# Kernel optimization log

Measured on AMD Instinct MI355X. Metric: run time of the kernel, lower is better.

Reference implementation:

```python
import jax, jax.numpy as jnp
import numpy as np

MASK_VALUE = 0.0  # default `mask=0` scalar in the original forward


def setup_inputs() -> dict:
    key = jax.random.key(0)
    kq, kk, kv = jax.random.split(key, 3)
    b, n, d_k, d_v = 8, 2048, 64, 64
    q = jax.random.normal(kq, (b, n, d_k), dtype=jnp.float32)
    k = jax.random.normal(kk, (b, n, d_k), dtype=jnp.float32)
    v = jax.random.normal(kv, (b, n, d_v), dtype=jnp.float32)
    return {"q": q, "k": k, "v": v}


def reference(q, k, v):
    d_k = q.shape[-1]
    temper = jnp.asarray(d_k, q.dtype) ** 0.5
    # scores: (b, n, n)
    attn = jnp.einsum('bqd,bkd->bqk', q, k) / temper
    # equality-based masking: positions whose score exactly equals the
    # scalar `mask` (default 0) are set to -inf before softmax.
    attn = jnp.where(attn == MASK_VALUE, -jnp.inf, attn)
    # NOTE: the original code calls `attn.masked_fill(look_ahead_mask==0, -inf)`
    # WITHOUT assignment, so the look-ahead mask is a no-op; we omit it faithfully.
    attn = jax.nn.softmax(attn, axis=-1)
    out = jnp.einsum('bqk,bkd->bqd', attn, v)  # (b, n, d_v)
    return out
```

## Files before the change

### kernel.cpp

```cpp
#include <hip/hip_runtime.h>
#include <hip/hip_bf16.h>

typedef __bf16 bf16_t;
typedef bf16_t bf16x2 __attribute__((ext_vector_type(2)));
typedef bf16_t bf16x8 __attribute__((ext_vector_type(8)));
typedef float  floatx4  __attribute__((ext_vector_type(4)));
typedef float  floatx16 __attribute__((ext_vector_type(16)));
typedef int    intx2    __attribute__((ext_vector_type(2)));

constexpr int B = 8, N = 2048, D = 64;

__global__ __launch_bounds__(256)
void prepass_kernel(const float* __restrict__ k, const float* __restrict__ v,
                    bf16_t* __restrict__ kf, bf16_t* __restrict__ vf) {
    __shared__ float t[32 * 65];
    const int tid = threadIdx.x;
    const int b   = blockIdx.x & 7;
    const int kvb = blockIdx.x >> 3;
    const size_t inoff  = ((size_t)b * N + kvb * 32) * D;
    const size_t outoff = (size_t)(b * 64 + kvb) * 2048;

    {
        const float* src = k + inoff;
        floatx4 f0 = *(const floatx4*)(src + tid * 8);
        floatx4 f1 = *(const floatx4*)(src + tid * 8 + 4);
        bf16x8 o;
        #pragma unroll
        for (int j = 0; j < 4; ++j) { o[j] = (bf16_t)f0[j]; o[j + 4] = (bf16_t)f1[j]; }
        const int rr = tid >> 3, kd = (tid >> 1) & 3, hh = tid & 1;
        *(bf16x8*)(kf + outoff + (size_t)kd * 512 + (hh * 32 + rr) * 8) = o;
    }
    {
        const float* src = v + inoff;
        floatx4 f0 = *(const floatx4*)(src + tid * 8);
        floatx4 f1 = *(const floatx4*)(src + tid * 8 + 4);
        const int rr = tid >> 3, cc = (tid & 7) * 8;
        #pragma unroll
        for (int j = 0; j < 4; ++j) { t[rr * 65 + cc + j] = f0[j]; t[rr * 65 + cc + 4 + j] = f1[j]; }
        __syncthreads();
        const int s2 = tid >> 7, dblk = (tid >> 6) & 1, lane = tid & 63;
        const int hh = lane >> 5, l31 = lane & 31;
        bf16x8 o;
        #pragma unroll
        for (int j = 0; j < 8; ++j)
            o[j] = (bf16_t)t[(s2 * 16 + hh * 8 + j) * 65 + dblk * 32 + l31];
        *(bf16x8*)(vf + outoff + (size_t)(s2 * 2 + dblk) * 512 + lane * 8) = o;
    }
}

__global__ __launch_bounds__(512, 4)
void attn_kernel(const float* __restrict__ q, const bf16_t* __restrict__ kf,
                 const bf16_t* __restrict__ vf, float* __restrict__ out) {
    __shared__ float o_buf[8 * 2048];
    __shared__ float l_buf[8 * 32];

    const int tid  = threadIdx.x;
    const int lane = tid & 63;
    const int cg   = tid >> 6;
    const int h    = lane >> 5;
    const int l31  = lane & 31;

    const int b  = blockIdx.x & 7;
    const int q0 = (blockIdx.x >> 3) * 32;

    const bf16_t* kfb = kf + (size_t)b * 131072;
    const bf16_t* vfb = vf + (size_t)b * 131072;

    constexpr float QSCALE = 0.125f * 1.4426950408889634f;
    bf16x8 qf[4];
    {
        const float* qp = q + ((size_t)b * N + q0 + l31) * D + h * 8;
        #pragma unroll
        for (int kd = 0; kd < 4; ++kd) {
            floatx4 f0 = *(const floatx4*)(qp + kd * 16);
            floatx4 f1 = *(const floatx4*)(qp + kd * 16 + 4);
            bf16x8 t;
            #pragma unroll
            for (int j = 0; j < 4; ++j) {
                t[j]     = (bf16_t)(f0[j] * QSCALE);
                t[j + 4] = (bf16_t)(f1[j] * QSCALE);
            }
            qf[kd] = t;
        }
    }

    floatx16 o_acc[2];
    #pragma unroll
    for (int d = 0; d < 2; ++d)
        #pragma unroll
        for (int i = 0; i < 16; ++i) o_acc[d][i] = 0.f;
    float l_run0 = 0.f, l_run1 = 0.f;

    bf16x8 kreg[4];
    #pragma unroll
    for (int kd = 0; kd < 4; ++kd)
        kreg[kd] = *(const bf16x8*)(kfb + (size_t)cg * 2048 + kd * 512 + lane * 8);

    #pragma unroll 2
    for (int it = 0; it < 8; ++it) {
        const size_t base = (size_t)(it * 8 + cg) * 2048;

        bf16x8 vreg[4];
        #pragma unroll
        for (int u = 0; u < 4; ++u)
            vreg[u] = *(const bf16x8*)(vfb + base + (size_t)u * 512 + lane * 8);

        floatx16 s;
        #pragma unroll
        for (int i = 0; i < 16; ++i) s[i] = 0.f;
        __builtin_amdgcn_s_setprio(1);
        #pragma unroll
        for (int kd = 0; kd < 4; ++kd)
            s = __builtin_amdgcn_mfma_f32_32x32x16_bf16(kreg[kd], qf[kd], s, 0, 0, 0);
        __builtin_amdgcn_s_setprio(0);

        if (it + 1 < 8) {
            const size_t nbase = (size_t)((it + 1) * 8 + cg) * 2048;
            #pragma unroll
            for (int kd = 0; kd < 4; ++kd)
                kreg[kd] = *(const bf16x8*)(kfb + nbase + (size_t)kd * 512 + lane * 8);
        }

        int q8[8];
        #pragma unroll
        for (int g = 0; g < 8; ++g) {
            union { int i; bf16x2 h2; } u;
            {
                float x = s[2 * g + 0];
                float p = (x == 0.0f) ? 0.0f : __builtin_amdgcn_exp2f(x);
                l_run0 += p;
                u.h2[0] = (bf16_t)p;
            }
            {
                float x = s[2 * g + 1];
                float p = (x == 0.0f) ? 0.0f : __builtin_amdgcn_exp2f(x);
                l_run1 += p;
                u.h2[1] = (bf16_t)p;
            }
            q8[g] = u.i;
        }

        #pragma unroll
        for (int s2 = 0; s2 < 2; ++s2) {
            intx2 p02 = __builtin_amdgcn_permlane32_swap(q8[4 * s2 + 0], q8[4 * s2 + 2], false, false);
            intx2 p13 = __builtin_amdgcn_permlane32_swap(q8[4 * s2 + 1], q8[4 * s2 + 3], false, false);
            union { int i4[4]; bf16x8 v; } bf;
            bf.i4[0] = p02[0];
            bf.i4[1] = p13[0];
            bf.i4[2] = p02[1];
            bf.i4[3] = p13[1];
            __builtin_amdgcn_s_setprio(1);
            #pragma unroll
            for (int dblk = 0; dblk < 2; ++dblk)
                o_acc[dblk] = __builtin_amdgcn_mfma_f32_32x32x16_bf16(vreg[s2 * 2 + dblk], bf.v,
                                                                      o_acc[dblk], 0, 0, 0);
            __builtin_amdgcn_s_setprio(0);
        }
    }

    float l_run = l_run0 + l_run1;
    l_run += __shfl_xor(l_run, 32);

    {
        float* ob = o_buf + cg * 2048;
        #pragma unroll
        for (int dblk = 0; dblk < 2; ++dblk)
            #pragma unroll
            for (int i = 0; i < 16; ++i) {
                const int d = (i & 3) + 8 * (i >> 2) + 4 * h + dblk * 32;
                ob[d * 32 + l31] = o_acc[dblk][i];
            }
        if (h == 0) l_buf[cg * 32 + l31] = l_run;
    }
    __syncthreads();
    {
        const int dblk = cg >> 2, g = cg & 3;
        const int d0 = 8 * g + 4 * h + dblk * 32;
        float lsum = 0.f;
        #pragma unroll
        for (int w = 0; w < 8; ++w) lsum += l_buf[w * 32 + l31];
        const float inv_l = 1.0f / lsum;
        floatx4 o4;
        #pragma unroll
        for (int j = 0; j < 4; ++j) {
            float sum = 0.f;
            #pragma unroll
            for (int w = 0; w < 8; ++w) sum += o_buf[w * 2048 + (d0 + j) * 32 + l31];
            o4[j] = sum * inv_l;
        }
        *(floatx4*)(out + ((size_t)b * N + q0 + l31) * D + d0) = o4;
    }
}

extern "C" void kernel_launch(void* const* d_in, const int* in_sizes, int n_in,
                              void* d_out, int out_size, void* d_ws, size_t ws_size,
                              hipStream_t stream) {
    const float* q = (const float*)d_in[0];
    const float* k = (const float*)d_in[1];
    const float* v = (const float*)d_in[2];
    float* out = (float*)d_out;
    bf16_t* kfrag = (bf16_t*)d_ws;
    bf16_t* vfrag = (bf16_t*)((char*)d_ws + (size_t)B * N * D * 2);

    hipLaunchKernelGGL(prepass_kernel, dim3(512), dim3(256), 0, stream, k, v, kfrag, vfrag);
    hipLaunchKernelGGL(attn_kernel, dim3(512), dim3(512), 0, stream, q, kfrag, vfrag, out);
}
```

Measured before the change: 80.68 us.

## Stream K/V tiles through LDS double buffer with global_load_lds and 4 waves

```diff
diff --git a/kernel.cpp b/kernel.cpp
--- a/kernel.cpp
+++ b/kernel.cpp
@@ -9,6 +9,12 @@
 typedef int    intx2    __attribute__((ext_vector_type(2)));
 
 constexpr int B = 8, N = 2048, D = 64;
+
+typedef __attribute__((address_space(1))) const void gconst_t;
+typedef __attribute__((address_space(3))) void lds_t;
+__device__ __forceinline__ void gload_lds16(const void* g, void* l) {
+    __builtin_amdgcn_global_load_lds((gconst_t*)g, (lds_t*)l, 16, 0, 0);
+}
 
 __global__ __launch_bounds__(256)
 void prepass_kernel(const float* __restrict__ k, const float* __restrict__ v,
@@ -48,11 +54,10 @@
     }
 }
 
-__global__ __launch_bounds__(512, 4)
+__global__ __launch_bounds__(256, 2)
 void attn_kernel(const float* __restrict__ q, const bf16_t* __restrict__ kf,
                  const bf16_t* __restrict__ vf, float* __restrict__ out) {
-    __shared__ float o_buf[8 * 2048];
-    __shared__ float l_buf[8 * 32];
+    __shared__ __align__(16) char smem[65536];
 
     const int tid  = threadIdx.x;
     const int lane = tid & 63;
@@ -63,8 +68,9 @@
     const int b  = blockIdx.x & 7;
     const int q0 = (blockIdx.x >> 3) * 32;
 
-    const bf16_t* kfb = kf + (size_t)b * 131072;
-    const bf16_t* vfb = vf + (size_t)b * 131072;
+    const char* kfb = (const char*)(kf + (size_t)b * 131072);
+    const char* vfb = (const char*)(vf + (size_t)b * 131072);
+    char* ring = smem + cg * 16384;
 
     constexpr float QSCALE = 0.125f * 1.4426950408889634f;
     bf16x8 qf[4];
@@ -84,6 +90,16 @@
         }
     }
 
+    {
+        const char* kc = kfb + (size_t)cg * 4096;
+        const char* vc = vfb + (size_t)cg * 4096;
+        #pragma unroll
+        for (int j = 0; j < 4; ++j) {
+            gload_lds16(kc + j * 1024 + lane * 16, ring + j * 1024);
+            gload_lds16(vc + j * 1024 + lane * 16, ring + 4096 + j * 1024);
+        }
+    }
+
     floatx16 o_acc[2];
     #pragma unroll
     for (int d = 0; d < 2; ++d)
@@ -91,19 +107,30 @@
         for (int i = 0; i < 16; ++i) o_acc[d][i] = 0.f;
     float l_run0 = 0.f, l_run1 = 0.f;
 
-    bf16x8 kreg[4];
     #pragma unroll
-    for (int kd = 0; kd < 4; ++kd)
-        kreg[kd] = *(const bf16x8*)(kfb + (size_t)cg * 2048 + kd * 512 + lane * 8);
-
-    #pragma unroll 2
-    for (int it = 0; it < 8; ++it) {
-        const size_t base = (size_t)(it * 8 + cg) * 2048;
-
-        bf16x8 vreg[4];
-        #pragma unroll
-        for (int u = 0; u < 4; ++u)
-            vreg[u] = *(const bf16x8*)(vfb + base + (size_t)u * 512 + lane * 8);
+    for (int it = 0; it < 16; ++it) {
+        char* cur = ring + (it & 1) * 8192;
+
+        if (it < 15) {
+            char* nxt = ring + ((it + 1) & 1) * 8192;
+            const char* kc = kfb + (size_t)((it + 1) * 4 + cg) * 4096;
+            const char* vc = vfb + (size_t)((it + 1) * 4 + cg) * 4096;
+            #pragma unroll
+            for (int j = 0; j < 4; ++j) {
+                gload_lds16(kc + j * 1024 + lane * 16, nxt + j * 1024);
+                gload_lds16(vc + j * 1024 + lane * 16, nxt + 4096 + j * 1024);
+            }
+            asm volatile("s_waitcnt vmcnt(8)" ::: "memory");
+        } else {
+            asm volatile("s_waitcnt vmcnt(0)" ::: "memory");
+        }
+
+        bf16x8 kreg[4], vreg[4];
+        #pragma unroll
+        for (int kd = 0; kd < 4; ++kd) {
+            kreg[kd] = *(const bf16x8*)(cur + kd * 1024 + lane * 16);
+            vreg[kd] = *(const bf16x8*)(cur + 4096 + kd * 1024 + lane * 16);
+        }
 
         floatx16 s;
         #pragma unroll
@@ -113,13 +140,6 @@
         for (int kd = 0; kd < 4; ++kd)
             s = __builtin_amdgcn_mfma_f32_32x32x16_bf16(kreg[kd], qf[kd], s, 0, 0, 0);
         __builtin_amdgcn_s_setprio(0);
-
-        if (it + 1 < 8) {
-            const size_t nbase = (size_t)((it + 1) * 8 + cg) * 2048;
-            #pragma unroll
-            for (int kd = 0; kd < 4; ++kd)
-                kreg[kd] = *(const bf16x8*)(kfb + nbase + (size_t)kd * 512 + lane * 8);
-        }
 
         int q8[8];
         #pragma unroll
@@ -162,7 +182,7 @@
     l_run += __shfl_xor(l_run, 32);
 
     {
-        float* ob = o_buf + cg * 2048;
+        float* ob = (float*)ring;
         #pragma unroll
         for (int dblk = 0; dblk < 2; ++dblk)
             #pragma unroll
@@ -170,25 +190,31 @@
                 const int d = (i & 3) + 8 * (i >> 2) + 4 * h + dblk * 32;
                 ob[d * 32 + l31] = o_acc[dblk][i];
             }
-        if (h == 0) l_buf[cg * 32 + l31] = l_run;
+        if (h == 0) ((float*)(ring + 8192))[l31] = l_run;
     }
     __syncthreads();
     {
-        const int dblk = cg >> 2, g = cg & 3;
-        const int d0 = 8 * g + 4 * h + dblk * 32;
+        const int mdblk = cg & 1;
+        const int g0 = (cg >> 1) * 2;
         float lsum = 0.f;
         #pragma unroll
-        for (int w = 0; w < 8; ++w) lsum += l_buf[w * 32 + l31];
+        for (int w = 0; w < 4; ++w) lsum += ((const float*)(smem + w * 16384 + 8192))[l31];
         const float inv_l = 1.0f / lsum;
-        floatx4 o4;
-        #pragma unroll
-        for (int j = 0; j < 4; ++j) {
-            float sum = 0.f;
-            #pragma unroll
-            for (int w = 0; w < 8; ++w) sum += o_buf[w * 2048 + (d0 + j) * 32 + l31];
-            o4[j] = sum * inv_l;
-        }
-        *(floatx4*)(out + ((size_t)b * N + q0 + l31) * D + d0) = o4;
+        float* op = out + ((size_t)b * N + q0 + l31) * D;
+        #pragma unroll
+        for (int gg = 0; gg < 2; ++gg) {
+            const int d0 = 8 * (g0 + gg) + 4 * h + mdblk * 32;
+            floatx4 o4;
+            #pragma unroll
+            for (int j = 0; j < 4; ++j) {
+                float sum = 0.f;
+                #pragma unroll
+                for (int w = 0; w < 4; ++w)
+                    sum += ((const float*)(smem + w * 16384))[(d0 + j) * 32 + l31];
+                o4[j] = sum * inv_l;
+            }
+            *(floatx4*)(op + d0) = o4;
+        }
     }
 }
 
@@ -203,5 +229,5 @@
     bf16_t* vfrag = (bf16_t*)((char*)d_ws + (size_t)B * N * D * 2);
 
     hipLaunchKernelGGL(prepass_kernel, dim3(512), dim3(256), 0, stream, k, v, kfrag, vfrag);
-    hipLaunchKernelGGL(attn_kernel, dim3(512), dim3(512), 0, stream, q, kfrag, vfrag, out);
-}
+    hipLaunchKernelGGL(attn_kernel, dim3(512), dim3(256), 0, stream, q, kfrag, vfrag, out);
+}
```

Measured after the change: 82.29 us. 1.02x slower.

## Process two 32-row query tiles per block to reuse K/V fragment loads

Applied to the files above, without the earlier changes.

```diff
diff --git a/kernel.cpp b/kernel.cpp
--- a/kernel.cpp
+++ b/kernel.cpp
@@ -48,11 +48,10 @@
     }
 }
 
-__global__ __launch_bounds__(512, 4)
+__global__ __launch_bounds__(512, 2)
 void attn_kernel(const float* __restrict__ q, const bf16_t* __restrict__ kf,
                  const bf16_t* __restrict__ vf, float* __restrict__ out) {
     __shared__ float o_buf[8 * 2048];
-    __shared__ float l_buf[8 * 32];
 
     const int tid  = threadIdx.x;
     const int lane = tid & 63;
@@ -61,35 +60,38 @@
     const int l31  = lane & 31;
 
     const int b  = blockIdx.x & 7;
-    const int q0 = (blockIdx.x >> 3) * 32;
+    const int q0 = (blockIdx.x >> 3) * 64;
 
     const bf16_t* kfb = kf + (size_t)b * 131072;
     const bf16_t* vfb = vf + (size_t)b * 131072;
 
     constexpr float QSCALE = 0.125f * 1.4426950408889634f;
-    bf16x8 qf[4];
-    {
-        const float* qp = q + ((size_t)b * N + q0 + l31) * D + h * 8;
+    bf16x8 qf[2][4];
+    #pragma unroll
+    for (int t = 0; t < 2; ++t) {
+        const float* qp = q + ((size_t)b * N + q0 + t * 32 + l31) * D + h * 8;
         #pragma unroll
         for (int kd = 0; kd < 4; ++kd) {
             floatx4 f0 = *(const floatx4*)(qp + kd * 16);
             floatx4 f1 = *(const floatx4*)(qp + kd * 16 + 4);
-            bf16x8 t;
+            bf16x8 tt;
             #pragma unroll
             for (int j = 0; j < 4; ++j) {
-                t[j]     = (bf16_t)(f0[j] * QSCALE);
-                t[j + 4] = (bf16_t)(f1[j] * QSCALE);
-            }
-            qf[kd] = t;
-        }
-    }
-
-    floatx16 o_acc[2];
-    #pragma unroll
-    for (int d = 0; d < 2; ++d)
-        #pragma unroll
-        for (int i = 0; i < 16; ++i) o_acc[d][i] = 0.f;
-    float l_run0 = 0.f, l_run1 = 0.f;
+                tt[j]     = (bf16_t)(f0[j] * QSCALE);
+                tt[j + 4] = (bf16_t)(f1[j] * QSCALE);
+            }
+            qf[t][kd] = tt;
+        }
+    }
+
+    floatx16 o_acc[2][2];
+    #pragma unroll
+    for (int t = 0; t < 2; ++t)
+        #pragma unroll
+        for (int d = 0; d < 2; ++d)
+            #pragma unroll
+            for (int i = 0; i < 16; ++i) o_acc[t][d][i] = 0.f;
+    float l_run[2][2] = {{0.f, 0.f}, {0.f, 0.f}};
 
     bf16x8 kreg[4];
     #pragma unroll
@@ -105,13 +107,18 @@
         for (int u = 0; u < 4; ++u)
             vreg[u] = *(const bf16x8*)(vfb + base + (size_t)u * 512 + lane * 8);
 
-        floatx16 s;
-        #pragma unroll
-        for (int i = 0; i < 16; ++i) s[i] = 0.f;
+        floatx16 s[2];
+        #pragma unroll
+        for (int t = 0; t < 2; ++t)
+            #pragma unroll
+            for (int i = 0; i < 16; ++i) s[t][i] = 0.f;
         __builtin_amdgcn_s_setprio(1);
         #pragma unroll
         for (int kd = 0; kd < 4; ++kd)
-            s = __builtin_amdgcn_mfma_f32_32x32x16_bf16(kreg[kd], qf[kd], s, 0, 0, 0);
+            s[0] = __builtin_amdgcn_mfma_f32_32x32x16_bf16(kreg[kd], qf[0][kd], s[0], 0, 0, 0);
+        #pragma unroll
+        for (int kd = 0; kd < 4; ++kd)
+            s[1] = __builtin_amdgcn_mfma_f32_32x32x16_bf16(kreg[kd], qf[1][kd], s[1], 0, 0, 0);
         __builtin_amdgcn_s_setprio(0);
 
         if (it + 1 < 8) {
@@ -121,74 +128,99 @@
                 kreg[kd] = *(const bf16x8*)(kfb + nbase + (size_t)kd * 512 + lane * 8);
         }
 
-        int q8[8];
-        #pragma unroll
-        for (int g = 0; g < 8; ++g) {
-            union { int i; bf16x2 h2; } u;
-            {
-                float x = s[2 * g + 0];
-                float p = (x == 0.0f) ? 0.0f : __builtin_amdgcn_exp2f(x);
-                l_run0 += p;
-                u.h2[0] = (bf16_t)p;
-            }
-            {
-                float x = s[2 * g + 1];
-                float p = (x == 0.0f) ? 0.0f : __builtin_amdgcn_exp2f(x);
-                l_run1 += p;
-                u.h2[1] = (bf16_t)p;
-            }
-            q8[g] = u.i;
-        }
-
-        #pragma unroll
-        for (int s2 = 0; s2 < 2; ++s2) {
-            intx2 p02 = __builtin_amdgcn_permlane32_swap(q8[4 * s2 + 0], q8[4 * s2 + 2], false, false);
-            intx2 p13 = __builtin_amdgcn_permlane32_swap(q8[4 * s2 + 1], q8[4 * s2 + 3], false, false);
-            union { int i4[4]; bf16x8 v; } bf;
-            bf.i4[0] = p02[0];
-            bf.i4[1] = p13[0];
-            bf.i4[2] = p02[1];
-            bf.i4[3] = p13[1];
-            __builtin_amdgcn_s_setprio(1);
+        #pragma unroll
+        for (int t = 0; t < 2; ++t) {
+            int q8[8];
+            #pragma unroll
+            for (int g = 0; g < 8; ++g) {
+                union { int i; bf16x2 h2; } u;
+                {
+                    float x = s[t][2 * g + 0];
+                    float p = (x == 0.0f) ? 0.0f : __builtin_amdgcn_exp2f(x);
+                    l_run[t][0] += p;
+                    u.h2[0] = (bf16_t)p;
+                }
+                {
+                    float x = s[t][2 * g + 1];
+                    float p = (x == 0.0f) ? 0.0f : __builtin_amdgcn_exp2f(x);
+                    l_run[t][1] += p;
+                    u.h2[1] = (bf16_t)p;
+                }
+                q8[g] = u.i;
+            }
+
+            #pragma unroll
+            for (int s2 = 0; s2 < 2; ++s2) {
+                intx2 p02 = __builtin_amdgcn_permlane32_swap(q8[4 * s2 + 0], q8[4 * s2 + 2], false, false);
+                intx2 p13 = __builtin_amdgcn_permlane32_swap(q8[4 * s2 + 1], q8[4 * s2 + 3], false, false);
+                union { int i4[4]; bf16x8 v; } bf;
+                bf.i4[0] = p02[0];
+                bf.i4[1] = p13[0];
+                bf.i4[2] = p02[1];
+                bf.i4[3] = p13[1];
+                __builtin_amdgcn_s_setprio(1);
+                #pragma unroll
+                for (int dblk = 0; dblk < 2; ++dblk)
+                    o_acc[t][dblk] = __builtin_amdgcn_mfma_f32_32x32x16_bf16(vreg[s2 * 2 + dblk], bf.v,
+                                                                             o_acc[t][dblk], 0, 0, 0);
+                __builtin_amdgcn_s_setprio(0);
+            }
+        }
+    }
+
+    #pragma unroll
+    for (int t = 0; t < 2; ++t) {
+        float l = l_run[t][0] + l_run[t][1];
+        l += __shfl_xor(l, 32);
+        l_run[t][0] = l;
+    }
+
+    if (h == 0) {
+        o_buf[cg * 32 + l31]       = l_run[0][0];
+        o_buf[256 + cg * 32 + l31] = l_run[1][0];
+    }
+    __syncthreads();
+    float inv_l[2];
+    {
+        float s0 = 0.f, s1 = 0.f;
+        #pragma unroll
+        for (int w = 0; w < 8; ++w) {
+            s0 += o_buf[w * 32 + l31];
+            s1 += o_buf[256 + w * 32 + l31];
+        }
+        inv_l[0] = 1.0f / s0;
+        inv_l[1] = 1.0f / s1;
+    }
+
+    #pragma unroll
+    for (int t = 0; t < 2; ++t) {
+        __syncthreads();
+        {
+            float* ob = o_buf + cg * 2048;
             #pragma unroll
             for (int dblk = 0; dblk < 2; ++dblk)
-                o_acc[dblk] = __builtin_amdgcn_mfma_f32_32x32x16_bf16(vreg[s2 * 2 + dblk], bf.v,
-                                                                      o_acc[dblk], 0, 0, 0);
-            __builtin_amdgcn_s_setprio(0);
-        }
-    }
-
-    float l_run = l_run0 + l_run1;
-    l_run += __shfl_xor(l_run, 32);
-
-    {
-        float* ob = o_buf + cg * 2048;
-        #pragma unroll
-        for (int dblk = 0; dblk < 2; ++dblk)
-            #pragma unroll
-            for (int i = 0; i < 16; ++i) {
-                const int d = (i & 3) + 8 * (i >> 2) + 4 * h + dblk * 32;
-                ob[d * 32 + l31] = o_acc[dblk][i];
-            }
-        if (h == 0) l_buf[cg * 32 + l31] = l_run;
-    }
-    __syncthreads();
-    {
-        const int dblk = cg >> 2, g = cg & 3;
-        const int d0 = 8 * g + 4 * h + dblk * 32;
-        float lsum = 0.f;
-        #pragma unroll
-        for (int w = 0; w < 8; ++w) lsum += l_buf[w * 32 + l31];
-        const float inv_l = 1.0f / lsum;
-        floatx4 o4;
-        #pragma unroll
-        for (int j = 0; j < 4; ++j) {
-            float sum = 0.f;
-            #pragma unroll
-            for (int w = 0; w < 8; ++w) sum += o_buf[w * 2048 + (d0 + j) * 32 + l31];
-            o4[j] = sum * inv_l;
-        }
-        *(floatx4*)(out + ((size_t)b * N + q0 + l31) * D + d0) = o4;
+                #pragma unroll
+                for (int i = 0; i < 16; ++i) {
+                    const int d = (i & 3) + 8 * (i >> 2) + 4 * h + dblk * 32;
+                    ob[d * 32 + l31] = o_acc[t][dblk][i];
+                }
+        }
+        __syncthreads();
+        {
+            const int mdblk = cg >> 2, g = cg & 3;
+            const int d0 = 8 * g + 4 * h + mdblk * 32;
+            float* op = out + ((size_t)b * N + q0 + t * 32 + l31) * D;
+            floatx4 o4;
+            #pragma unroll
+            for (int j = 0; j < 4; ++j) {
+                float sum = 0.f;
+                #pragma unroll
+                for (int w = 0; w < 8; ++w)
+                    sum += o_buf[w * 2048 + (d0 + j) * 32 + l31];
+                o4[j] = sum * inv_l[t];
+            }
+            *(floatx4*)(op + d0) = o4;
+        }
     }
 }
 
@@ -203,5 +235,5 @@
     bf16_t* vfrag = (bf16_t*)((char*)d_ws + (size_t)B * N * D * 2);
 
     hipLaunchKernelGGL(prepass_kernel, dim3(512), dim3(256), 0, stream, k, v, kfrag, vfrag);
-    hipLaunchKernelGGL(attn_kernel, dim3(512), dim3(512), 0, stream, q, kfrag, vfrag, out);
+    hipLaunchKernelGGL(attn_kernel, dim3(256), dim3(512), 0, stream, q, kfrag, vfrag, out);
 }
```

After: 82.43 us. +2.2%, slower.
